# Optimization experiments

Measured on AMD Instinct MI355X. Metric: run time of the kernel, lower is better.

Reference implementation:

```python
import jax, jax.numpy as jnp
import numpy as np

B, S, K, N = 4, 2048, 4096, 4096
QMAX = 127.0  # symmetric int8 range used by protoquant qntz


def setup_inputs() -> dict:
    key = jax.random.key(0)
    k1, k2, k3, k4 = jax.random.split(key, 4)
    inp = jax.random.normal(k1, (B, S, K), dtype=jnp.float32)
    # int8 quantized weight, already transposed to [K, N] as in self.qweight_transposed
    qweight_t = jax.random.randint(k2, (K, N), -127, 128, dtype=jnp.int8)
    # per-output-channel dequant scale (wparams)
    wscale = jax.random.uniform(k3, (N,), dtype=jnp.float32, minval=0.001, maxval=0.02)
    bias = jax.random.normal(k4, (N,), dtype=jnp.float32)
    return {"inp": inp, "qweight_t": qweight_t, "wscale": wscale, "bias": bias}


def reference(inp, qweight_t, wscale, bias):
    Bb, Ss, Kk = inp.shape
    x = inp.reshape(Bb * Ss, Kk)  # [M, K]
    # qntz(inp, is_a=True): dynamic per-row symmetric int8 quantization
    amax = jnp.max(jnp.abs(x), axis=1, keepdims=True)  # [M, 1]
    iscale = amax / QMAX                               # per-row dequant scale
    q = jnp.clip(jnp.round(x / jnp.maximum(iscale, 1e-12)), -QMAX, QMAX).astype(jnp.int8)
    d = jnp.matmul(q, qweight_t, preferred_element_type=jnp.int32)  # [M, N]
    # dqntz: scale rows by activation scale, cols by weight scale, add bias
    out = d.astype(jnp.float32) * iscale * wscale[None, :] + bias[None, :]
    return out.reshape(Bb, Ss, -1)
```

## Files before the change

kernel.cpp:

```cpp
#include <hip/hip_runtime.h>

#define M_DIM 8192
#define N_DIM 4096
#define K_DIM 4096

typedef __attribute__((ext_vector_type(4))) int i32x4;

__device__ __forceinline__ void gload_lds16(const void* g, void* l) {
  __builtin_amdgcn_global_load_lds(
      (const __attribute__((address_space(1))) void*)g,
      (__attribute__((address_space(3))) void*)l, 16, 0, 0);
}

#define MFMA_I8(a, b, c) __builtin_amdgcn_mfma_i32_16x16x64_i8((a), (b), (c), 0, 0, 0)

__global__ __launch_bounds__(256) void quant_rows(const float* __restrict__ x,
                                                  signed char* __restrict__ q,
                                                  float* __restrict__ iscale) {
  const int row = blockIdx.x;
  const int t = threadIdx.x;
  const float* xr = x + (size_t)row * K_DIM;
  float4 v[4];
  float vmax = 0.f;
#pragma unroll
  for (int i = 0; i < 4; ++i) {
    v[i] = reinterpret_cast<const float4*>(xr)[t + i * 256];
    vmax = fmaxf(vmax, fmaxf(fmaxf(fabsf(v[i].x), fabsf(v[i].y)),
                             fmaxf(fabsf(v[i].z), fabsf(v[i].w))));
  }
#pragma unroll
  for (int off = 32; off > 0; off >>= 1)
    vmax = fmaxf(vmax, __shfl_xor(vmax, off));
  __shared__ float smax[4];
  if ((t & 63) == 0) smax[t >> 6] = vmax;
  __syncthreads();
  vmax = fmaxf(fmaxf(smax[0], smax[1]), fmaxf(smax[2], smax[3]));
  const float isc = vmax * (1.0f / 127.0f);
  if (t == 0) iscale[row] = isc;
  const float s = fmaxf(isc, 1e-12f);
  unsigned* qrow = reinterpret_cast<unsigned*>(q + (size_t)row * K_DIM);
#pragma unroll
  for (int i = 0; i < 4; ++i) {
    int b0 = (int)rintf(fminf(fmaxf(v[i].x / s, -127.f), 127.f));
    int b1 = (int)rintf(fminf(fmaxf(v[i].y / s, -127.f), 127.f));
    int b2 = (int)rintf(fminf(fmaxf(v[i].z / s, -127.f), 127.f));
    int b3 = (int)rintf(fminf(fmaxf(v[i].w / s, -127.f), 127.f));
    qrow[t + i * 256] = (unsigned)(b0 & 0xff) | ((unsigned)(b1 & 0xff) << 8) |
                        ((unsigned)(b2 & 0xff) << 16) |
                        ((unsigned)(b3 & 0xff) << 24);
  }
}

__global__ __launch_bounds__(256) void transpose_w8(const int* __restrict__ w,
                                                    signed char* __restrict__ wt) {
  __shared__ signed char tile[64][68];
  const int n0 = blockIdx.x * 64;
  const int k0 = blockIdx.y * 64;
  const int t = threadIdx.x;
#pragma unroll
  for (int i = 0; i < 4; ++i) {
    int idx = t + i * 256;
    int r = idx >> 4;
    int c = idx & 15;
    int4 v = *reinterpret_cast<const int4*>(w + (size_t)(k0 + r) * N_DIM + n0 + c * 4);
    unsigned dw = (unsigned)(v.x & 0xff) | ((unsigned)(v.y & 0xff) << 8) |
                  ((unsigned)(v.z & 0xff) << 16) | ((unsigned)(v.w & 0xff) << 24);
    *reinterpret_cast<unsigned*>(&tile[r][c * 4]) = dw;
  }
  __syncthreads();
#pragma unroll
  for (int i = 0; i < 4; ++i) {
    int idx = t + i * 256;
    int n = idx >> 4;
    int kd = idx & 15;
    unsigned b0 = (unsigned char)tile[kd * 4 + 0][n];
    unsigned b1 = (unsigned char)tile[kd * 4 + 1][n];
    unsigned b2 = (unsigned char)tile[kd * 4 + 2][n];
    unsigned b3 = (unsigned char)tile[kd * 4 + 3][n];
    unsigned dw = b0 | (b1 << 8) | (b2 << 16) | (b3 << 24);
    *reinterpret_cast<unsigned*>(wt + (size_t)(n0 + n) * K_DIM + k0 + kd * 4) = dw;
  }
}

#define BM 256
#define BN 256
#define BK 128
#define NKT (K_DIM / BK)

__global__ __launch_bounds__(512, 2) void gemm_i8(
    const signed char* __restrict__ q,
    const signed char* __restrict__ wt,
    const float* __restrict__ iscale,
    const float* __restrict__ wscale,
    const float* __restrict__ bias,
    float* __restrict__ out)
{
  __shared__ __align__(16) signed char lA[2][BM * BK];
  __shared__ __align__(16) signed char lB[2][BN * BK];

  const int t = threadIdx.x;
  const int l = t & 63;
  const int wid = t >> 6;
  const int wm = wid >> 2;
  const int wn = wid & 3;
  const int fl = l & 15;
  const int fk = l >> 4;
  const int ps0 = fk ^ (fl & 7);
  const int ps1 = (4 + fk) ^ (fl & 7);

  const int lin = blockIdx.y * 16 + blockIdx.x;
  const int swz = (lin & 7) * 64 + (lin >> 3);
  const int m0 = (swz >> 4) * BM;
  const int n0 = (swz & 15) * BN;

  const int srow = t >> 3;
  const int ss = t & 7;
  const unsigned gss = (unsigned)((ss ^ (srow & 7)) << 4);
  const int a0r = srow, a1r = 128 + srow, a2r = 64 + srow, a3r = 192 + srow;
  const int blr = ((srow >> 5) << 6) + (srow & 31);
  const int b0r = blr, b1r = 128 + blr, b2r = 32 + blr, b3r = 160 + blr;

  const unsigned goA0 = (unsigned)(m0 + a0r) * K_DIM + gss;
  const unsigned goA1 = (unsigned)(m0 + a1r) * K_DIM + gss;
  const unsigned goA2 = (unsigned)(m0 + a2r) * K_DIM + gss;
  const unsigned goA3 = (unsigned)(m0 + a3r) * K_DIM + gss;
  const unsigned goB0 = (unsigned)(n0 + b0r) * K_DIM + gss;
  const unsigned goB1 = (unsigned)(n0 + b1r) * K_DIM + gss;
  const unsigned goB2 = (unsigned)(n0 + b2r) * K_DIM + gss;
  const unsigned goB3 = (unsigned)(n0 + b3r) * K_DIM + gss;
  const int loA0 = a0r * BK + (ss << 4), loA1 = a1r * BK + (ss << 4);
  const int loA2 = a2r * BK + (ss << 4), loA3 = a3r * BK + (ss << 4);
  const int loB0 = b0r * BK + (ss << 4), loB1 = b1r * BK + (ss << 4);
  const int loB2 = b2r * BK + (ss << 4), loB3 = b3r * BK + (ss << 4);

  i32x4 acc[8][4] = {};
  i32x4 af[4][2], bf0[2][2], bf1[2][2];

  gload_lds16(q + goA0, &lA[0][0] + loA0);
  gload_lds16(q + goA1, &lA[0][0] + loA1);
  gload_lds16(wt + goB0, &lB[0][0] + loB0);
  gload_lds16(wt + goB1, &lB[0][0] + loB1);
  gload_lds16(wt + goB2, &lB[0][0] + loB2);
  gload_lds16(wt + goB3, &lB[0][0] + loB3);
  gload_lds16(q + goA2, &lA[0][0] + loA2);
  gload_lds16(q + goA3, &lA[0][0] + loA3);
  asm volatile("s_waitcnt vmcnt(4)" ::: "memory");
  __builtin_amdgcn_s_barrier();

  for (int kt = 0; kt < NKT; ++kt) {
    const int cur = kt & 1;
    const signed char* lAc = &lA[cur][0];
    const signed char* lBc = &lB[cur][0];
    signed char* lAn = &lA[cur ^ 1][0];
    signed char* lBn = &lB[cur ^ 1][0];
    const unsigned kbn = (unsigned)(((kt + 1) & (NKT - 1)) * BK);

#pragma unroll
    for (int mi = 0; mi < 4; ++mi) {
      const int row = wm * 128 + mi * 16 + fl;
      af[mi][0] = *(const i32x4*)(lAc + row * BK + ps0 * 16);
      af[mi][1] = *(const i32x4*)(lAc + row * BK + ps1 * 16);
    }
#pragma unroll
    for (int ni = 0; ni < 2; ++ni) {
      const int row = wn * 64 + ni * 16 + fl;
      bf0[ni][0] = *(const i32x4*)(lBc + row * BK + ps0 * 16);
      bf0[ni][1] = *(const i32x4*)(lBc + row * BK + ps1 * 16);
    }
    gload_lds16(q + (goA0 + kbn), lAn + loA0);
    gload_lds16(q + (goA1 + kbn), lAn + loA1);
    asm volatile("s_waitcnt lgkmcnt(0)" ::: "memory");
    __builtin_amdgcn_sched_barrier(0);
    __builtin_amdgcn_s_setprio(1);
#pragma unroll
    for (int mi = 0; mi < 4; ++mi)
#pragma unroll
      for (int ni = 0; ni < 2; ++ni) {
        acc[mi][ni] = MFMA_I8(af[mi][0], bf0[ni][0], acc[mi][ni]);
        acc[mi][ni] = MFMA_I8(af[mi][1], bf0[ni][1], acc[mi][ni]);
      }
    __builtin_amdgcn_s_setprio(0);
    asm volatile("s_waitcnt vmcnt(4)" ::: "memory");
    __builtin_amdgcn_s_barrier();

#pragma unroll
    for (int ni = 0; ni < 2; ++ni) {
      const int row = wn * 64 + 32 + ni * 16 + fl;
      bf1[ni][0] = *(const i32x4*)(lBc + row * BK + ps0 * 16);
      bf1[ni][1] = *(const i32x4*)(lBc + row * BK + ps1 * 16);
    }
    gload_lds16(wt + (goB0 + kbn), lBn + loB0);
    gload_lds16(wt + (goB1 + kbn), lBn + loB1);
    asm volatile("s_waitcnt lgkmcnt(0)" ::: "memory");
    __builtin_amdgcn_sched_barrier(0);
    __builtin_amdgcn_s_setprio(1);
#pragma unroll
    for (int mi = 0; mi < 4; ++mi)
#pragma unroll
      for (int ni = 0; ni < 2; ++ni) {
        acc[mi][2 + ni] = MFMA_I8(af[mi][0], bf1[ni][0], acc[mi][2 + ni]);
        acc[mi][2 + ni] = MFMA_I8(af[mi][1], bf1[ni][1], acc[mi][2 + ni]);
      }
    __builtin_amdgcn_s_setprio(0);
    asm volatile("s_waitcnt vmcnt(4)" ::: "memory");
    __builtin_amdgcn_s_barrier();

#pragma unroll
    for (int mi = 0; mi < 4; ++mi) {
      const int row = wm * 128 + 64 + mi * 16 + fl;
      af[mi][0] = *(const i32x4*)(lAc + row * BK + ps0 * 16);
      af[mi][1] = *(const i32x4*)(lAc + row * BK + ps1 * 16);
    }
    gload_lds16(wt + (goB2 + kbn), lBn + loB2);
    gload_lds16(wt + (goB3 + kbn), lBn + loB3);
    gload_lds16(q + (goA2 + kbn), lAn + loA2);
    gload_lds16(q + (goA3 + kbn), lAn + loA3);
    asm volatile("s_waitcnt lgkmcnt(0)" ::: "memory");
    __builtin_amdgcn_sched_barrier(0);
    __builtin_amdgcn_s_setprio(1);
#pragma unroll
    for (int mi = 0; mi < 4; ++mi)
#pragma unroll
      for (int ni = 0; ni < 2; ++ni) {
        acc[4 + mi][2 + ni] = MFMA_I8(af[mi][0], bf1[ni][0], acc[4 + mi][2 + ni]);
        acc[4 + mi][2 + ni] = MFMA_I8(af[mi][1], bf1[ni][1], acc[4 + mi][2 + ni]);
      }
#pragma unroll
    for (int mi = 0; mi < 4; ++mi)
#pragma unroll
      for (int ni = 0; ni < 2; ++ni) {
        acc[4 + mi][ni] = MFMA_I8(af[mi][0], bf0[ni][0], acc[4 + mi][ni]);
        acc[4 + mi][ni] = MFMA_I8(af[mi][1], bf0[ni][1], acc[4 + mi][ni]);
      }
    __builtin_amdgcn_s_setprio(0);
    asm volatile("s_waitcnt vmcnt(4)" ::: "memory");
    __builtin_amdgcn_s_barrier();
  }

  const int colb = n0 + wn * 64 + fl;
  const int rowb = m0 + wm * 128 + fk * 4;
#pragma unroll
  for (int mi = 0; mi < 8; ++mi) {
    const int rowoff = ((mi >> 2) * 64 + (mi & 3) * 16);
    float is4[4];
#pragma unroll
    for (int r = 0; r < 4; ++r) is4[r] = iscale[rowb + rowoff + r];
#pragma unroll
    for (int ni = 0; ni < 4; ++ni) {
      const int col = colb + (ni >> 1) * 32 + (ni & 1) * 16;
      const float wsc = wscale[col];
      const float bs = bias[col];
#pragma unroll
      for (int r = 0; r < 4; ++r) {
        out[(size_t)(rowb + rowoff + r) * N_DIM + col] =
            (float)acc[mi][ni][r] * is4[r] * wsc + bs;
      }
    }
  }
}

extern "C" void kernel_launch(void* const* d_in, const int* in_sizes, int n_in,
                              void* d_out, int out_size, void* d_ws, size_t ws_size,
                              hipStream_t stream) {
  const float* inp = (const float*)d_in[0];
  const int* wq32 = (const int*)d_in[1];
  const float* wscale = (const float*)d_in[2];
  const float* bias = (const float*)d_in[3];
  float* out = (float*)d_out;

  signed char* q = (signed char*)d_ws;
  signed char* wt = q + (size_t)M_DIM * K_DIM;
  float* iscale = (float*)(wt + (size_t)N_DIM * K_DIM);

  quant_rows<<<M_DIM, 256, 0, stream>>>(inp, q, iscale);
  transpose_w8<<<dim3(N_DIM / 64, K_DIM / 64), 256, 0, stream>>>(wq32, wt);
  gemm_i8<<<dim3(N_DIM / BN, M_DIM / BM), 512, 0, stream>>>(q, wt, iscale, wscale,
                                                            bias, out);
}
```

Baseline: 182.5 us.

## Double-buffer A fragments and prefetch next tile's A rows during MFMA phases

Splits the A fragment registers into two sets (af0/af1). The first A half for the next k-tile is now read from the other LDS buffer in the last phase, and the second half is read earlier, alongside the bf1 MFMAs. This moves LDS fragment loads off the head of each phase so they overlap MFMA work. The vmcnt waits are tightened to 2 so the A rows of the next buffer are guaranteed resident before they are prefetched. It costs extra VGPRs, which may hurt occupancy or cause spills.

```diff
diff --git a/kernel.cpp b/kernel.cpp
--- a/kernel.cpp
+++ b/kernel.cpp
@@ -134,7 +134,7 @@
   const int loB2 = b2r * BK + (ss << 4), loB3 = b3r * BK + (ss << 4);
 
   i32x4 acc[8][4] = {};
-  i32x4 af[4][2], bf0[2][2], bf1[2][2];
+  i32x4 af0[4][2], af1[4][2], bf0[2][2], bf1[2][2];
 
   gload_lds16(q + goA0, &lA[0][0] + loA0);
   gload_lds16(q + goA1, &lA[0][0] + loA1);
@@ -146,6 +146,12 @@
   gload_lds16(q + goA3, &lA[0][0] + loA3);
   asm volatile("s_waitcnt vmcnt(4)" ::: "memory");
   __builtin_amdgcn_s_barrier();
+#pragma unroll
+  for (int mi = 0; mi < 4; ++mi) {
+    const int row = wm * 128 + mi * 16 + fl;
+    af0[mi][0] = *(const i32x4*)(&lA[0][0] + row * BK + ps0 * 16);
+    af0[mi][1] = *(const i32x4*)(&lA[0][0] + row * BK + ps1 * 16);
+  }
 
   for (int kt = 0; kt < NKT; ++kt) {
     const int cur = kt & 1;
@@ -156,12 +162,6 @@
     const unsigned kbn = (unsigned)(((kt + 1) & (NKT - 1)) * BK);
 
 #pragma unroll
-    for (int mi = 0; mi < 4; ++mi) {
-      const int row = wm * 128 + mi * 16 + fl;
-      af[mi][0] = *(const i32x4*)(lAc + row * BK + ps0 * 16);
-      af[mi][1] = *(const i32x4*)(lAc + row * BK + ps1 * 16);
-    }
-#pragma unroll
     for (int ni = 0; ni < 2; ++ni) {
       const int row = wn * 64 + ni * 16 + fl;
       bf0[ni][0] = *(const i32x4*)(lBc + row * BK + ps0 * 16);
@@ -176,11 +176,11 @@
     for (int mi = 0; mi < 4; ++mi)
 #pragma unroll
       for (int ni = 0; ni < 2; ++ni) {
-        acc[mi][ni] = MFMA_I8(af[mi][0], bf0[ni][0], acc[mi][ni]);
-        acc[mi][ni] = MFMA_I8(af[mi][1], bf0[ni][1], acc[mi][ni]);
-      }
-    __builtin_amdgcn_s_setprio(0);
-    asm volatile("s_waitcnt vmcnt(4)" ::: "memory");
+        acc[mi][ni] = MFMA_I8(af0[mi][0], bf0[ni][0], acc[mi][ni]);
+        acc[mi][ni] = MFMA_I8(af0[mi][1], bf0[ni][1], acc[mi][ni]);
+      }
+    __builtin_amdgcn_s_setprio(0);
+    asm volatile("s_waitcnt vmcnt(2)" ::: "memory");
     __builtin_amdgcn_s_barrier();
 
 #pragma unroll
@@ -195,22 +195,22 @@
     __builtin_amdgcn_sched_barrier(0);
     __builtin_amdgcn_s_setprio(1);
 #pragma unroll
-    for (int mi = 0; mi < 4; ++mi)
-#pragma unroll
-      for (int ni = 0; ni < 2; ++ni) {
-        acc[mi][2 + ni] = MFMA_I8(af[mi][0], bf1[ni][0], acc[mi][2 + ni]);
-        acc[mi][2 + ni] = MFMA_I8(af[mi][1], bf1[ni][1], acc[mi][2 + ni]);
-      }
-    __builtin_amdgcn_s_setprio(0);
-    asm volatile("s_waitcnt vmcnt(4)" ::: "memory");
-    __builtin_amdgcn_s_barrier();
-
-#pragma unroll
     for (int mi = 0; mi < 4; ++mi) {
       const int row = wm * 128 + 64 + mi * 16 + fl;
-      af[mi][0] = *(const i32x4*)(lAc + row * BK + ps0 * 16);
-      af[mi][1] = *(const i32x4*)(lAc + row * BK + ps1 * 16);
-    }
+      af1[mi][0] = *(const i32x4*)(lAc + row * BK + ps0 * 16);
+      af1[mi][1] = *(const i32x4*)(lAc + row * BK + ps1 * 16);
+    }
+#pragma unroll
+    for (int mi = 0; mi < 4; ++mi)
+#pragma unroll
+      for (int ni = 0; ni < 2; ++ni) {
+        acc[mi][2 + ni] = MFMA_I8(af0[mi][0], bf1[ni][0], acc[mi][2 + ni]);
+        acc[mi][2 + ni] = MFMA_I8(af0[mi][1], bf1[ni][1], acc[mi][2 + ni]);
+      }
+    __builtin_amdgcn_s_setprio(0);
+    asm volatile("s_waitcnt vmcnt(2)" ::: "memory");
+    __builtin_amdgcn_s_barrier();
+
     gload_lds16(wt + (goB2 + kbn), lBn + loB2);
     gload_lds16(wt + (goB3 + kbn), lBn + loB3);
     gload_lds16(q + (goA2 + kbn), lAn + loA2);
@@ -222,15 +222,24 @@
     for (int mi = 0; mi < 4; ++mi)
 #pragma unroll
       for (int ni = 0; ni < 2; ++ni) {
-        acc[4 + mi][2 + ni] = MFMA_I8(af[mi][0], bf1[ni][0], acc[4 + mi][2 + ni]);
-        acc[4 + mi][2 + ni] = MFMA_I8(af[mi][1], bf1[ni][1], acc[4 + mi][2 + ni]);
-      }
-#pragma unroll
-    for (int mi = 0; mi < 4; ++mi)
-#pragma unroll
-      for (int ni = 0; ni < 2; ++ni) {
-        acc[4 + mi][ni] = MFMA_I8(af[mi][0], bf0[ni][0], acc[4 + mi][ni]);
-        acc[4 + mi][ni] = MFMA_I8(af[mi][1], bf0[ni][1], acc[4 + mi][ni]);
+        acc[4 + mi][2 + ni] = MFMA_I8(af1[mi][0], bf1[ni][0], acc[4 + mi][2 + ni]);
+        acc[4 + mi][2 + ni] = MFMA_I8(af1[mi][1], bf1[ni][1], acc[4 + mi][2 + ni]);
+      }
+    __builtin_amdgcn_s_setprio(0);
+#pragma unroll
+    for (int mi = 0; mi < 4; ++mi) {
+      const int row = wm * 128 + mi * 16 + fl;
+      af0[mi][0] = *(const i32x4*)(lAn + row * BK + ps0 * 16);
+      af0[mi][1] = *(const i32x4*)(lAn + row * BK + ps1 * 16);
+    }
+    __builtin_amdgcn_sched_barrier(0);
+    __builtin_amdgcn_s_setprio(1);
+#pragma unroll
+    for (int mi = 0; mi < 4; ++mi)
+#pragma unroll
+      for (int ni = 0; ni < 2; ++ni) {
+        acc[4 + mi][ni] = MFMA_I8(af1[mi][0], bf0[ni][0], acc[4 + mi][ni]);
+        acc[4 + mi][ni] = MFMA_I8(af1[mi][1], bf0[ni][1], acc[4 + mi][ni]);
       }
     __builtin_amdgcn_s_setprio(0);
     asm volatile("s_waitcnt vmcnt(4)" ::: "memory");
```

After: 200.3 us. 1.1x slower.
